# Optimization experiments

Hardware: AMD Instinct MI355X
Metric: run time of the kernel (lower is better)

## Reference

```python
import jax, jax.numpy as jnp
import numpy as np

B, T, D = 2, 2048, 1024
H = 16
HD = D // H
WINDOW = 128
N_GLOBAL = 1
SCALE = 1.0 / np.sqrt(HD)


def _attend_mask(T):
    # True = allowed to attend: banded local window + global rows/cols
    idx = jnp.arange(T)
    dist = jnp.abs(idx[:, None] - idx[None, :])
    attend = dist <= WINDOW
    glb = idx < N_GLOBAL
    attend = attend | glb[:, None] | glb[None, :]
    return attend  # [T, T] bool


def setup_inputs() -> dict:
    key = jax.random.key(0)
    ks = jax.random.split(key, 5)
    scale_w = 1.0 / np.sqrt(D)
    return {
        "x": jax.random.normal(ks[0], (B, T, D), dtype=jnp.float32),
        "Wq": jax.random.normal(ks[1], (D, D), dtype=jnp.float32) * scale_w,
        "Wk": jax.random.normal(ks[2], (D, D), dtype=jnp.float32) * scale_w,
        "Wv": jax.random.normal(ks[3], (D, D), dtype=jnp.float32) * scale_w,
        "Wo": jax.random.normal(ks[4], (D, D), dtype=jnp.float32) * scale_w,
    }


def reference(x, Wq, Wk, Wv, Wo):
    Bb, Tt, Dd = x.shape
    # torch nn.Linear: y = x @ W.T
    q = (x @ Wq.T).reshape(Bb, Tt, H, HD).transpose(0, 2, 1, 3)  # [B,H,T,hd]
    k = (x @ Wk.T).reshape(Bb, Tt, H, HD).transpose(0, 2, 1, 3)
    v = (x @ Wv.T).reshape(Bb, Tt, H, HD).transpose(0, 2, 1, 3)

    attend = _attend_mask(Tt)  # [T,T]
    logits = jnp.einsum("bhqd,bhkd->bhqk", q, k) * SCALE
    logits = jnp.where(attend[None, None, :, :], logits, -jnp.inf)
    weights = jax.nn.softmax(logits, axis=-1)
    weights = jnp.nan_to_num(weights)
    out = jnp.einsum("bhqk,bhkd->bhqd", weights, v)
    out = out.transpose(0, 2, 1, 3).reshape(Bb, Tt, Dd)
    return out @ Wo.T
```

## Files before the change

### kernel.cpp

```cpp
#include <hip/hip_runtime.h>

typedef unsigned short u16;
typedef __attribute__((ext_vector_type(8))) __bf16 bf16x8;
typedef __attribute__((ext_vector_type(4))) float f32x4;
typedef __attribute__((ext_vector_type(8))) u16 u16x8;

#define T_SEQ 2048
#define DIM   1024
#define HDIM  64
#define WIN   128
#define XN_EL (2 * T_SEQ * DIM)

#define AS1 __attribute__((address_space(1)))
#define AS3 __attribute__((address_space(3)))

__device__ __forceinline__ u16 f2bf(float f) {
  union { float f; unsigned u; } v; v.f = f;
  unsigned r = v.u + 0x7fffu + ((v.u >> 16) & 1u);
  return (u16)(r >> 16);
}
__device__ __forceinline__ float bf2f(u16 u) {
  union { unsigned u; float f; } v; v.u = ((unsigned)u) << 16; return v.f;
}
__device__ __forceinline__ void bar() {
  asm volatile("" ::: "memory");
  __builtin_amdgcn_s_barrier();
  asm volatile("" ::: "memory");
}

__global__ __launch_bounds__(256) void cvt_all(
    const float* __restrict__ x,  const float* __restrict__ wq,
    const float* __restrict__ wk, const float* __restrict__ wv,
    const float* __restrict__ wo, u16* __restrict__ xb, u16* __restrict__ wb) {
  const int bid = blockIdx.x;
  const float* s;
  u16* d;
  int off;
  if (bid < 2048) {
    s = x; d = xb; off = bid * 2048;
  } else {
    const int w = bid - 2048;
    const int m = w >> 9;
    s = (m == 0) ? wq : ((m == 1) ? wk : ((m == 2) ? wv : wo));
    d = wb + ((size_t)m << 20);
    off = (w & 511) * 2048;
  }
  const int i = off + threadIdx.x * 8;
  const float4* s4 = (const float4*)(s + i);
  float4 a = s4[0], b = s4[1];
  u16x8 r;
  r[0] = f2bf(a.x); r[1] = f2bf(a.y); r[2] = f2bf(a.z); r[3] = f2bf(a.w);
  r[4] = f2bf(b.x); r[5] = f2bf(b.y); r[6] = f2bf(b.z); r[7] = f2bf(b.w);
  *(u16x8*)(d + i) = r;
}

template <int BM, int BN, int WM, int WN, int OS, int SPLIT, typename OUT_T>
__global__ __launch_bounds__(WM * WN * 64, 2) void gemm3(
    const u16* __restrict__ A, const u16* __restrict__ B,
    OUT_T* __restrict__ C, int nbm) {
  constexpr int NW = WM * WN;
  constexpr int RM = BM / WM, RN = BN / WN;
  constexpr int MF = RM / 16, NF = RN / 16;
  constexpr int MPH = MF / 4;
  constexpr int NT = DIM / 64;
  constexpr int CA = BM / 8, CB = BN / 8;
  constexpr int ANW = CA / NW;
  constexpr int BNW = CB / NW;

  __shared__ u16 As[2][BM * 64];
  __shared__ u16 Bs[2][BN * 64];

  const int tid = threadIdx.x;
  const int lane = tid & 63;
  const int wid = tid >> 6;
  const int wr = wid / WN, wc = wid % WN;
  const int c15 = lane & 15, g = lane >> 4;
  const int lr = lane >> 3;
  const int lcs = ((lane & 7) ^ lr) << 3;

  const int cpx = gridDim.x >> 3;
  const int bid = ((int)blockIdx.x & 7) * cpx + ((int)blockIdx.x >> 3);
  const int bm = bid % nbm;
  const int nb = bid / nbm;
  const u16* Ab = A + (size_t)bm * BM * DIM;
  const u16* Bb = B + (size_t)nb * BN * DIM;

  f32x4 acc[MF][NF];
#pragma unroll
  for (int m = 0; m < MF; ++m)
#pragma unroll
    for (int n = 0; n < NF; ++n) acc[m][n] = (f32x4){0.f, 0.f, 0.f, 0.f};

  auto stA = [&](int buf, int half, int k0) {
#pragma unroll
    for (int i = 0; i < ANW / 2; ++i) {
      const int c = half * (CA / 2) + wid * (ANW / 2) + i;
      __builtin_amdgcn_global_load_lds(
          (const AS1 void*)(Ab + (size_t)(c * 8 + lr) * DIM + k0 + lcs),
          (AS3 void*)(&As[buf][c * 512]), 16, 0, 0);
    }
  };
  auto stB = [&](int buf, int k0) {
#pragma unroll
    for (int i = 0; i < BNW; ++i) {
      const int c = wid * BNW + i;
      __builtin_amdgcn_global_load_lds(
          (const AS1 void*)(Bb + (size_t)(c * 8 + lr) * DIM + k0 + lcs),
          (AS3 void*)(&Bs[buf][c * 512]), 16, 0, 0);
    }
  };

  stA(0, 0, 0); stA(0, 1, 0);
  stB(0, 0); stB(1, 64);
  if constexpr (BNW == 3) asm volatile("s_waitcnt vmcnt(3)" ::: "memory");
  else                    asm volatile("s_waitcnt vmcnt(4)" ::: "memory");
  bar();

  for (int t = 0; t < NT; ++t) {
    const int buf = t & 1;
    const int k0 = t * 64;
    bf16x8 bfrag[NF][2];
#pragma unroll
    for (int p = 0; p < 4; ++p) {
      if (p == 0) {
#pragma unroll
        for (int n = 0; n < NF; ++n)
#pragma unroll
          for (int ks = 0; ks < 2; ++ks) {
            const int r = wc * RN + n * 16 + c15;
            bfrag[n][ks] = *(const bf16x8*)(
                &Bs[buf][r * 64 + ((ks * 32 + g * 8) ^ ((r & 7) << 3))]);
          }
      }
      bf16x8 af[MPH][2];
#pragma unroll
      for (int m = 0; m < MPH; ++m)
#pragma unroll
        for (int ks = 0; ks < 2; ++ks) {
          const int r = wr * RM + (p * MPH + m) * 16 + c15;
          af[m][ks] = *(const bf16x8*)(
              &As[buf][r * 64 + ((ks * 32 + g * 8) ^ ((r & 7) << 3))]);
        }
      if (p == 0) {
        if (t + 1 < NT) stA(buf ^ 1, 0, k0 + 64);
      } else if (p == 1) {
        if (t + 1 < NT) stA(buf ^ 1, 1, k0 + 64);
      } else if (p == 2) {
        if (t + 2 < NT) stB(buf, k0 + 128);
      } else {
        if (t < NT - 2) {
          if constexpr (BNW == 3) asm volatile("s_waitcnt vmcnt(3)" ::: "memory");
          else                    asm volatile("s_waitcnt vmcnt(4)" ::: "memory");
        } else {
          asm volatile("s_waitcnt vmcnt(0)" ::: "memory");
        }
      }
      bar();
      __builtin_amdgcn_s_setprio(1);
#pragma unroll
      for (int m = 0; m < MPH; ++m)
#pragma unroll
        for (int n = 0; n < NF; ++n)
#pragma unroll
          for (int ks = 0; ks < 2; ++ks)
            acc[p * MPH + m][n] = __builtin_amdgcn_mfma_f32_16x16x32_bf16(
                af[m][ks], bfrag[n][ks], acc[p * MPH + m][n], 0, 0, 0);
      __builtin_amdgcn_s_setprio(0);
      bar();
    }
  }

#pragma unroll
  for (int m = 0; m < MF; ++m) {
    const int row0 = bm * BM + wr * RM + m * 16 + g * 4;
#pragma unroll
    for (int n = 0; n < NF; ++n) {
      const int col = nb * BN + wc * RN + n * 16 + c15;
#pragma unroll
      for (int j = 0; j < 4; ++j) {
        if constexpr (SPLIT) {
          u16* dst = (u16*)C + (size_t)(col >> 10) * (size_t)XN_EL +
                     (col & 1023) + (size_t)(row0 + j) * DIM;
          *dst = f2bf(acc[m][n][j]);
        } else {
          const size_t idx = (size_t)(row0 + j) * OS + col;
          if constexpr (sizeof(OUT_T) == 2) C[idx] = f2bf(acc[m][n][j]);
          else C[idx] = acc[m][n][j];
        }
      }
    }
  }
}

__global__ __launch_bounds__(256) void sparse_attn(
    const u16* __restrict__ Q, const u16* __restrict__ K,
    const u16* __restrict__ V, u16* __restrict__ AO) {
  __shared__ u16 Ks[64 * 72];
  __shared__ u16 Vt[64 * 72];
  __shared__ u16 Pl[4][16 * 72];
  __shared__ float Pg[4][16];

  const int tid = threadIdx.x;
  const int lane = tid & 63;
  const int wid = tid >> 6;
  const size_t ha = (size_t)blockIdx.z * T_SEQ * DIM + (size_t)blockIdx.y * HDIM;
  const u16* Qp = Q + ha;
  const u16* Kp = K + ha;
  const u16* Vp = V + ha;

  if (blockIdx.x == 32) {
    float* qs   = (float*)Pg;
    float* ps   = (float*)Ks;
    float* rbuf = (float*)Vt;
    float* red  = (float*)Pl;

    if (tid < HDIM) qs[tid] = bf2f(Qp[tid]);
    __syncthreads();

    float lsum = 0.f;
#pragma unroll
    for (int j = 0; j < 8; ++j) {
      const int k = tid + 256 * j;
      const u16* kr = Kp + (size_t)k * DIM;
      float acc = 0.f;
#pragma unroll
      for (int d0 = 0; d0 < 8; ++d0) {
        u16x8 kv = *(const u16x8*)(kr + d0 * 8);
#pragma unroll
        for (int e = 0; e < 8; ++e) acc += qs[d0 * 8 + e] * bf2f(kv[e]);
      }
      const float p = __expf(acc * 0.125f);
      ps[k] = p;
      lsum += p;
    }
#pragma unroll
    for (int s = 1; s < 64; s <<= 1) lsum += __shfl_xor(lsum, s);
    if (lane == 0) red[wid] = lsum;
    __syncthreads();
    const float denom = red[0] + red[1] + red[2] + red[3];

    const int kg = tid >> 3, dg = tid & 7;
    float facc[8] = {0.f, 0.f, 0.f, 0.f, 0.f, 0.f, 0.f, 0.f};
#pragma unroll 8
    for (int i = 0; i < 64; ++i) {
      const int k = kg * 64 + i;
      const u16x8 vv = *(const u16x8*)(Vp + (size_t)k * DIM + dg * 8);
      const float p = ps[k];
#pragma unroll
      for (int e = 0; e < 8; ++e) facc[e] += p * bf2f(vv[e]);
    }
#pragma unroll
    for (int e = 0; e < 8; ++e) rbuf[kg * 64 + dg * 8 + e] = facc[e];
    __syncthreads();
    if (tid < HDIM) {
      float tot = 0.f;
#pragma unroll
      for (int k2 = 0; k2 < 32; ++k2) tot += rbuf[k2 * 64 + tid];
      AO[ha + tid] = f2bf(tot / denom);
    }
    return;
  }

  const int c15 = lane & 15;
  const int g = lane >> 4;
  const int q0 = blockIdx.x * 64;

  bf16x8 qf0, qf1;
  {
    const u16* qp = Qp + (size_t)(q0 + wid * 16 + c15) * DIM + g * 8;
    qf0 = *(const bf16x8*)qp;
    qf1 = *(const bf16x8*)(qp + 32);
  }

  float lrun[4] = {0.f, 0.f, 0.f, 0.f};
  f32x4 ao[4];
#pragma unroll
  for (int c = 0; c < 4; ++c) ao[c] = (f32x4){0.f, 0.f, 0.f, 0.f};

  const int klo = (q0 > WIN) ? (q0 - WIN) : 0;
  int khi = q0 + 64 + WIN;
  if (khi > T_SEQ) khi = T_SEQ;
  const int nt = (khi - klo) >> 6;

  const int srr = tid >> 2;
  const int scc = (tid & 3) * 16;
  const int vr = srr ^ ((scc >> 4) << 4);

  const u16* kbase = Kp + (size_t)(klo + srr) * DIM + scc;
  const u16* vbase = Vp + (size_t)(klo + srr) * DIM + scc;
  u16x8 kp0 = *(const u16x8*)kbase;
  u16x8 kp1 = *(const u16x8*)(kbase + 8);
  u16x8 vp0 = *(const u16x8*)vbase;
  u16x8 vp1 = *(const u16x8*)(vbase + 8);

  for (int ti = 0; ti < nt; ++ti) {
    const int kt = klo + ti * 64;
    *(u16x8*)(Ks + srr * 72 + scc) = kp0;
    *(u16x8*)(Ks + srr * 72 + scc + 8) = kp1;
#pragma unroll
    for (int e = 0; e < 8; ++e) {
      Vt[(scc + e) * 72 + vr] = vp0[e];
      Vt[(scc + 8 + e) * 72 + vr] = vp1[e];
    }
    __syncthreads();

    if (ti + 1 < nt) {
      const u16* kn = kbase + (size_t)(ti + 1) * 64 * DIM;
      const u16* vn = vbase + (size_t)(ti + 1) * 64 * DIM;
      kp0 = *(const u16x8*)kn;
      kp1 = *(const u16x8*)(kn + 8);
      vp0 = *(const u16x8*)vn;
      vp1 = *(const u16x8*)(vn + 8);
    }

    f32x4 s[4];
#pragma unroll
    for (int t = 0; t < 4; ++t) {
      const u16* kr = Ks + (t * 16 + c15) * 72 + g * 8;
      bf16x8 ka = *(const bf16x8*)kr;
      bf16x8 kb = *(const bf16x8*)(kr + 32);
      s[t] = (f32x4){0.f, 0.f, 0.f, 0.f};
      s[t] = __builtin_amdgcn_mfma_f32_16x16x32_bf16(qf0, ka, s[t], 0, 0, 0);
      s[t] = __builtin_amdgcn_mfma_f32_16x16x32_bf16(qf1, kb, s[t], 0, 0, 0);
    }
#pragma unroll
    for (int j = 0; j < 4; ++j) {
      const int qg = q0 + wid * 16 + g * 4 + j;
#pragma unroll
      for (int t = 0; t < 4; ++t) {
        const int kg = kt + t * 16 + c15;
        const int dd = qg - kg;
        const bool ok = (kg == 0) || (dd <= WIN && dd >= -WIN);
        const float p = ok ? __expf(s[t][j] * 0.125f) : 0.f;
        lrun[j] += p;
        Pl[wid][(g * 4 + j) * 72 + t * 16 + c15] = f2bf(p);
      }
    }
    asm volatile("s_waitcnt lgkmcnt(0)" ::: "memory");

    const bf16x8 pa0 = *(const bf16x8*)(&Pl[wid][c15 * 72 + g * 8]);
    const bf16x8 pa1 = *(const bf16x8*)(&Pl[wid][c15 * 72 + 32 + g * 8]);
#pragma unroll
    for (int c = 0; c < 4; ++c) {
      const int rb = (c * 16 + c15) * 72;
      bf16x8 va = *(const bf16x8*)(Vt + rb + ((g * 8) ^ (c << 4)));
      bf16x8 vb = *(const bf16x8*)(Vt + rb + ((32 + g * 8) ^ (c << 4)));
      ao[c] = __builtin_amdgcn_mfma_f32_16x16x32_bf16(pa0, va, ao[c], 0, 0, 0);
      ao[c] = __builtin_amdgcn_mfma_f32_16x16x32_bf16(pa1, vb, ao[c], 0, 0, 0);
    }
    __syncthreads();
  }

  float ltot[4];
#pragma unroll
  for (int j = 0; j < 4; ++j) {
    float ls = lrun[j];
    ls += __shfl_xor(ls, 1);
    ls += __shfl_xor(ls, 2);
    ls += __shfl_xor(ls, 4);
    ls += __shfl_xor(ls, 8);
    ltot[j] = ls;
  }

  if (klo > 0) {
    const u16x8 qu0 = *(const u16x8*)&qf0;
    const u16x8 qu1 = *(const u16x8*)&qf1;
    const u16x8 k0a = *(const u16x8*)(Kp + g * 8);
    const u16x8 k0b = *(const u16x8*)(Kp + 32 + g * 8);
    float sg = 0.f;
#pragma unroll
    for (int e = 0; e < 8; ++e)
      sg += bf2f(qu0[e]) * bf2f(k0a[e]) + bf2f(qu1[e]) * bf2f(k0b[e]);
    sg += __shfl_xor(sg, 16);
    sg += __shfl_xor(sg, 32);
    const float pg = __expf(sg * 0.125f);
    Pg[wid][c15] = pg;
    asm volatile("s_waitcnt lgkmcnt(0)" ::: "memory");
#pragma unroll
    for (int j = 0; j < 4; ++j) {
      const float pj = Pg[wid][g * 4 + j];
      ltot[j] += pj;
#pragma unroll
      for (int c = 0; c < 4; ++c)
        ao[c][j] += pj * bf2f(Vp[c * 16 + c15]);
    }
  }

#pragma unroll
  for (int j = 0; j < 4; ++j) {
    const int qrow = q0 + wid * 16 + g * 4 + j;
    if (qrow == 0) continue;
    const float inv = 1.0f / ltot[j];
#pragma unroll
    for (int c = 0; c < 4; ++c)
      AO[ha + (size_t)qrow * DIM + c * 16 + c15] = f2bf(ao[c][j] * inv);
  }
}

extern "C" void kernel_launch(void* const* d_in, const int* in_sizes, int n_in,
                              void* d_out, int out_size, void* d_ws, size_t ws_size,
                              hipStream_t stream) {
  const float* x  = (const float*)d_in[0];
  const float* Wq = (const float*)d_in[1];
  const float* Wk = (const float*)d_in[2];
  const float* Wv = (const float*)d_in[3];
  const float* Wo = (const float*)d_in[4];
  float* out = (float*)d_out;

  const int WN = DIM * DIM;

  u16* ws  = (u16*)d_ws;
  u16* xb  = ws;
  u16* wb  = ws + (size_t)XN_EL;
  u16* Wob = wb + (size_t)3 * WN;
  u16* Qb  = wb + (size_t)4 * WN;
  u16* Kb  = Qb + (size_t)XN_EL;
  u16* Vb  = Kb + (size_t)XN_EL;

  cvt_all<<<4096, 256, 0, stream>>>(x, Wq, Wk, Wv, Wo, xb, wb);

  gemm3<256, 192, 2, 4, DIM, 1, u16><<<256, 512, 0, stream>>>(xb, wb, Qb, 16);

  sparse_attn<<<dim3(33, 16, 2), 256, 0, stream>>>(Qb, Kb, Vb, xb);

  gemm3<128, 128, 2, 2, DIM, 0, float><<<256, 256, 0, stream>>>(xb, Wob, out, 32);
}
```

Before: 106.6 us.

## Write V transposed from QKV GEMM and double-buffer attention tiles via direct LDS loads

The QKV GEMM epilogue now writes V head-transposed ([b,h,d,t]), so the attention kernel no longer transposes V through scalar LDS stores. K and V tiles are staged with global_load_lds into double-buffered, XOR-swizzled LDS, which replaces the register prefetch. A fast path skips the mask computation for tiles that lie fully inside the window. The global-row reduction is reworked to read the transposed V. The risks are more LDS use, a stride-T scattered epilogue store for V, and a swizzle that has to match between the direct-load and read patterns.

```diff
diff --git a/kernel.cpp b/kernel.cpp
--- a/kernel.cpp
+++ b/kernel.cpp
@@ -4,6 +4,7 @@
 typedef __attribute__((ext_vector_type(8))) __bf16 bf16x8;
 typedef __attribute__((ext_vector_type(4))) float f32x4;
 typedef __attribute__((ext_vector_type(8))) u16 u16x8;
+typedef __attribute__((ext_vector_type(4))) u16 u16x4;
 
 #define T_SEQ 2048
 #define DIM   1024
@@ -176,13 +177,26 @@
 #pragma unroll
     for (int n = 0; n < NF; ++n) {
       const int col = nb * BN + wc * RN + n * 16 + c15;
-#pragma unroll
-      for (int j = 0; j < 4; ++j) {
-        if constexpr (SPLIT) {
-          u16* dst = (u16*)C + (size_t)(col >> 10) * (size_t)XN_EL +
-                     (col & 1023) + (size_t)(row0 + j) * DIM;
-          *dst = f2bf(acc[m][n][j]);
+      if constexpr (SPLIT) {
+        if (col < 2048) {
+#pragma unroll
+          for (int j = 0; j < 4; ++j) {
+            u16* dst = (u16*)C + (size_t)(col >> 10) * (size_t)XN_EL +
+                       (col & 1023) + (size_t)(row0 + j) * DIM;
+            *dst = f2bf(acc[m][n][j]);
+          }
         } else {
+          const int h = (col - 2048) >> 6, dd = (col - 2048) & 63;
+          u16x4 pk;
+#pragma unroll
+          for (int j = 0; j < 4; ++j) pk[j] = f2bf(acc[m][n][j]);
+          const size_t vidx =
+              ((size_t)((row0 >> 11) * 16 + h) * 64 + dd) * T_SEQ + (row0 & 2047);
+          *(u16x4*)((u16*)C + (size_t)2 * XN_EL + vidx) = pk;
+        }
+      } else {
+#pragma unroll
+        for (int j = 0; j < 4; ++j) {
           const size_t idx = (size_t)(row0 + j) * OS + col;
           if constexpr (sizeof(OUT_T) == 2) C[idx] = f2bf(acc[m][n][j]);
           else C[idx] = acc[m][n][j];
@@ -194,9 +208,9 @@
 
 __global__ __launch_bounds__(256) void sparse_attn(
     const u16* __restrict__ Q, const u16* __restrict__ K,
-    const u16* __restrict__ V, u16* __restrict__ AO) {
-  __shared__ u16 Ks[64 * 72];
-  __shared__ u16 Vt[64 * 72];
+    const u16* __restrict__ VT, u16* __restrict__ AO) {
+  __shared__ u16 Kt[2][64 * 64];
+  __shared__ u16 Vt[2][64 * 64];
   __shared__ u16 Pl[4][16 * 72];
   __shared__ float Pg[4][16];
 
@@ -204,15 +218,16 @@
   const int lane = tid & 63;
   const int wid = tid >> 6;
   const size_t ha = (size_t)blockIdx.z * T_SEQ * DIM + (size_t)blockIdx.y * HDIM;
+  const size_t hv = ((size_t)blockIdx.z * 16 + blockIdx.y) * HDIM * T_SEQ;
   const u16* Qp = Q + ha;
   const u16* Kp = K + ha;
-  const u16* Vp = V + ha;
+  const u16* Vp = VT + hv;
 
   if (blockIdx.x == 32) {
-    float* qs   = (float*)Pg;
-    float* ps   = (float*)Ks;
-    float* rbuf = (float*)Vt;
-    float* red  = (float*)Pl;
+    float* qs   = (float*)Pl;
+    float* ps   = (float*)(&Kt[0][0]);
+    float* rbuf = (float*)(&Vt[0][0]);
+    float* red  = (float*)Pg;
 
     if (tid < HDIM) qs[tid] = bf2f(Qp[tid]);
     __syncthreads();
@@ -239,23 +254,19 @@
     __syncthreads();
     const float denom = red[0] + red[1] + red[2] + red[3];
 
-    const int kg = tid >> 3, dg = tid & 7;
-    float facc[8] = {0.f, 0.f, 0.f, 0.f, 0.f, 0.f, 0.f, 0.f};
-#pragma unroll 8
-    for (int i = 0; i < 64; ++i) {
-      const int k = kg * 64 + i;
-      const u16x8 vv = *(const u16x8*)(Vp + (size_t)k * DIM + dg * 8);
-      const float p = ps[k];
-#pragma unroll
-      for (int e = 0; e < 8; ++e) facc[e] += p * bf2f(vv[e]);
-    }
-#pragma unroll
-    for (int e = 0; e < 8; ++e) rbuf[kg * 64 + dg * 8 + e] = facc[e];
+    const int d = tid & 63, kc = tid >> 6;
+    const u16* vr = Vp + (size_t)d * T_SEQ + kc * 512;
+    float facc = 0.f;
+#pragma unroll 4
+    for (int i = 0; i < 512; i += 8) {
+      const u16x8 vv = *(const u16x8*)(vr + i);
+#pragma unroll
+      for (int e = 0; e < 8; ++e) facc += ps[kc * 512 + i + e] * bf2f(vv[e]);
+    }
+    rbuf[kc * 64 + d] = facc;
     __syncthreads();
     if (tid < HDIM) {
-      float tot = 0.f;
-#pragma unroll
-      for (int k2 = 0; k2 < 32; ++k2) tot += rbuf[k2 * 64 + tid];
+      const float tot = rbuf[tid] + rbuf[64 + tid] + rbuf[128 + tid] + rbuf[192 + tid];
       AO[ha + tid] = f2bf(tot / denom);
     }
     return;
@@ -282,58 +293,64 @@
   if (khi > T_SEQ) khi = T_SEQ;
   const int nt = (khi - klo) >> 6;
 
-  const int srr = tid >> 2;
-  const int scc = (tid & 3) * 16;
-  const int vr = srr ^ ((scc >> 4) << 4);
-
-  const u16* kbase = Kp + (size_t)(klo + srr) * DIM + scc;
-  const u16* vbase = Vp + (size_t)(klo + srr) * DIM + scc;
-  u16x8 kp0 = *(const u16x8*)kbase;
-  u16x8 kp1 = *(const u16x8*)(kbase + 8);
-  u16x8 vp0 = *(const u16x8*)vbase;
-  u16x8 vp1 = *(const u16x8*)(vbase + 8);
+  const int lr = lane >> 3;
+  const int lcs = ((lane & 7) ^ lr) << 3;
+
+  auto stage = [&](int buf, int kt) {
+#pragma unroll
+    for (int i = 0; i < 2; ++i) {
+      const int c = wid * 2 + i;
+      __builtin_amdgcn_global_load_lds(
+          (const AS1 void*)(Kp + (size_t)(kt + c * 8 + lr) * DIM + lcs),
+          (AS3 void*)(&Kt[buf][c * 512]), 16, 0, 0);
+      __builtin_amdgcn_global_load_lds(
+          (const AS1 void*)(Vp + (size_t)(c * 8 + lr) * T_SEQ + kt + lcs),
+          (AS3 void*)(&Vt[buf][c * 512]), 16, 0, 0);
+    }
+  };
+
+  stage(0, klo);
+  asm volatile("s_waitcnt vmcnt(0)" ::: "memory");
+  __syncthreads();
 
   for (int ti = 0; ti < nt; ++ti) {
     const int kt = klo + ti * 64;
-    *(u16x8*)(Ks + srr * 72 + scc) = kp0;
-    *(u16x8*)(Ks + srr * 72 + scc + 8) = kp1;
-#pragma unroll
-    for (int e = 0; e < 8; ++e) {
-      Vt[(scc + e) * 72 + vr] = vp0[e];
-      Vt[(scc + 8 + e) * 72 + vr] = vp1[e];
-    }
-    __syncthreads();
-
-    if (ti + 1 < nt) {
-      const u16* kn = kbase + (size_t)(ti + 1) * 64 * DIM;
-      const u16* vn = vbase + (size_t)(ti + 1) * 64 * DIM;
-      kp0 = *(const u16x8*)kn;
-      kp1 = *(const u16x8*)(kn + 8);
-      vp0 = *(const u16x8*)vn;
-      vp1 = *(const u16x8*)(vn + 8);
-    }
+    const int buf = ti & 1;
+    if (ti + 1 < nt) stage(buf ^ 1, kt + 64);
 
     f32x4 s[4];
 #pragma unroll
     for (int t = 0; t < 4; ++t) {
-      const u16* kr = Ks + (t * 16 + c15) * 72 + g * 8;
-      bf16x8 ka = *(const bf16x8*)kr;
-      bf16x8 kb = *(const bf16x8*)(kr + 32);
+      const int r = t * 16 + c15;
+      bf16x8 ka = *(const bf16x8*)(&Kt[buf][r * 64 + ((g * 8) ^ ((r & 7) << 3))]);
+      bf16x8 kb = *(const bf16x8*)(&Kt[buf][r * 64 + ((32 + g * 8) ^ ((r & 7) << 3))]);
       s[t] = (f32x4){0.f, 0.f, 0.f, 0.f};
       s[t] = __builtin_amdgcn_mfma_f32_16x16x32_bf16(qf0, ka, s[t], 0, 0, 0);
       s[t] = __builtin_amdgcn_mfma_f32_16x16x32_bf16(qf1, kb, s[t], 0, 0, 0);
     }
-#pragma unroll
-    for (int j = 0; j < 4; ++j) {
-      const int qg = q0 + wid * 16 + g * 4 + j;
-#pragma unroll
-      for (int t = 0; t < 4; ++t) {
-        const int kg = kt + t * 16 + c15;
-        const int dd = qg - kg;
-        const bool ok = (kg == 0) || (dd <= WIN && dd >= -WIN);
-        const float p = ok ? __expf(s[t][j] * 0.125f) : 0.f;
-        lrun[j] += p;
-        Pl[wid][(g * 4 + j) * 72 + t * 16 + c15] = f2bf(p);
+    if (kt >= q0 - 65 && kt <= q0 + 65) {
+#pragma unroll
+      for (int j = 0; j < 4; ++j) {
+#pragma unroll
+        for (int t = 0; t < 4; ++t) {
+          const float p = __expf(s[t][j] * 0.125f);
+          lrun[j] += p;
+          Pl[wid][(g * 4 + j) * 72 + t * 16 + c15] = f2bf(p);
+        }
+      }
+    } else {
+#pragma unroll
+      for (int j = 0; j < 4; ++j) {
+        const int qg = q0 + wid * 16 + g * 4 + j;
+#pragma unroll
+        for (int t = 0; t < 4; ++t) {
+          const int kg = kt + t * 16 + c15;
+          const int dd = qg - kg;
+          const bool ok = (kg == 0) || (dd <= WIN && dd >= -WIN);
+          const float p = ok ? __expf(s[t][j] * 0.125f) : 0.f;
+          lrun[j] += p;
+          Pl[wid][(g * 4 + j) * 72 + t * 16 + c15] = f2bf(p);
+        }
       }
     }
     asm volatile("s_waitcnt lgkmcnt(0)" ::: "memory");
@@ -342,9 +359,9 @@
     const bf16x8 pa1 = *(const bf16x8*)(&Pl[wid][c15 * 72 + 32 + g * 8]);
 #pragma unroll
     for (int c = 0; c < 4; ++c) {
-      const int rb = (c * 16 + c15) * 72;
-      bf16x8 va = *(const bf16x8*)(Vt + rb + ((g * 8) ^ (c << 4)));
-      bf16x8 vb = *(const bf16x8*)(Vt + rb + ((32 + g * 8) ^ (c << 4)));
+      const int r = c * 16 + c15;
+      bf16x8 va = *(const bf16x8*)(&Vt[buf][r * 64 + ((g * 8) ^ ((r & 7) << 3))]);
+      bf16x8 vb = *(const bf16x8*)(&Vt[buf][r * 64 + ((32 + g * 8) ^ ((r & 7) << 3))]);
       ao[c] = __builtin_amdgcn_mfma_f32_16x16x32_bf16(pa0, va, ao[c], 0, 0, 0);
       ao[c] = __builtin_amdgcn_mfma_f32_16x16x32_bf16(pa1, vb, ao[c], 0, 0, 0);
     }
@@ -382,7 +399,7 @@
       ltot[j] += pj;
 #pragma unroll
       for (int c = 0; c < 4; ++c)
-        ao[c][j] += pj * bf2f(Vp[c * 16 + c15]);
+        ao[c][j] += pj * bf2f(Vp[(size_t)(c * 16 + c15) * T_SEQ]);
     }
   }
 
@@ -415,13 +432,13 @@
   u16* Wob = wb + (size_t)3 * WN;
   u16* Qb  = wb + (size_t)4 * WN;
   u16* Kb  = Qb + (size_t)XN_EL;
-  u16* Vb  = Kb + (size_t)XN_EL;
+  u16* VTb = Qb + (size_t)2 * XN_EL;
 
   cvt_all<<<4096, 256, 0, stream>>>(x, Wq, Wk, Wv, Wo, xb, wb);
 
   gemm3<256, 192, 2, 4, DIM, 1, u16><<<256, 512, 0, stream>>>(xb, wb, Qb, 16);
 
-  sparse_attn<<<dim3(33, 16, 2), 256, 0, stream>>>(Qb, Kb, Vb, xb);
+  sparse_attn<<<dim3(33, 16, 2), 256, 0, stream>>>(Qb, Kb, VTb, xb);
 
   gemm3<128, 128, 2, 2, DIM, 0, float><<<256, 256, 0, stream>>>(xb, Wob, out, 32);
 }
```

New measurement: 114.7 us. +7.6%, slower.

## Process 128 query rows per attention block and skip masking on interior tiles

Applied to the files above, without the earlier changes.

Each attention block now covers 128 queries instead of 64, with every wave handling two 16-row groups. Each staged K/V tile in shared memory is therefore reused by twice as many queries, which cuts redundant global loads of the overlapping window. The grid shrinks from 33 to 17 blocks per head. A fast path also drops the per-element mask test when the tile lies entirely inside the band. The cost is fewer blocks, and so less parallelism and latency hiding, plus higher register pressure from the doubled accumulators.

```diff
diff --git a/kernel.cpp b/kernel.cpp
--- a/kernel.cpp
+++ b/kernel.cpp
@@ -198,7 +198,7 @@
   __shared__ u16 Ks[64 * 72];
   __shared__ u16 Vt[64 * 72];
   __shared__ u16 Pl[4][16 * 72];
-  __shared__ float Pg[4][16];
+  __shared__ float Pg[4][32];
 
   const int tid = threadIdx.x;
   const int lane = tid & 63;
@@ -208,11 +208,11 @@
   const u16* Kp = K + ha;
   const u16* Vp = V + ha;
 
-  if (blockIdx.x == 32) {
-    float* qs   = (float*)Pg;
+  if (blockIdx.x == 16) {
+    float* qs   = (float*)(&Pl[0][0]);
     float* ps   = (float*)Ks;
     float* rbuf = (float*)Vt;
-    float* red  = (float*)Pl;
+    float* red  = (float*)Pg;
 
     if (tid < HDIM) qs[tid] = bf2f(Qp[tid]);
     __syncthreads();
@@ -263,28 +263,35 @@
 
   const int c15 = lane & 15;
   const int g = lane >> 4;
-  const int q0 = blockIdx.x * 64;
-
-  bf16x8 qf0, qf1;
+  const int q0 = blockIdx.x * 128;
+  const int qw = q0 + wid * 32;
+
+  bf16x8 qA0, qA1, qB0, qB1;
   {
-    const u16* qp = Qp + (size_t)(q0 + wid * 16 + c15) * DIM + g * 8;
-    qf0 = *(const bf16x8*)qp;
-    qf1 = *(const bf16x8*)(qp + 32);
-  }
-
-  float lrun[4] = {0.f, 0.f, 0.f, 0.f};
-  f32x4 ao[4];
-#pragma unroll
-  for (int c = 0; c < 4; ++c) ao[c] = (f32x4){0.f, 0.f, 0.f, 0.f};
+    const u16* qp = Qp + (size_t)(qw + c15) * DIM + g * 8;
+    qA0 = *(const bf16x8*)qp;
+    qA1 = *(const bf16x8*)(qp + 32);
+    const u16* qp2 = qp + 16 * DIM;
+    qB0 = *(const bf16x8*)qp2;
+    qB1 = *(const bf16x8*)(qp2 + 32);
+  }
+
+  float lrA[4] = {0.f, 0.f, 0.f, 0.f}, lrB[4] = {0.f, 0.f, 0.f, 0.f};
+  f32x4 aoA[4], aoB[4];
+#pragma unroll
+  for (int c = 0; c < 4; ++c) {
+    aoA[c] = (f32x4){0.f, 0.f, 0.f, 0.f};
+    aoB[c] = (f32x4){0.f, 0.f, 0.f, 0.f};
+  }
 
   const int klo = (q0 > WIN) ? (q0 - WIN) : 0;
-  int khi = q0 + 64 + WIN;
+  int khi = q0 + 128 + WIN;
   if (khi > T_SEQ) khi = T_SEQ;
   const int nt = (khi - klo) >> 6;
 
   const int srr = tid >> 2;
   const int scc = (tid & 3) * 16;
-  const int vr = srr ^ ((scc >> 4) << 4);
+  const int vr = srr ^ (scc & 48);
 
   const u16* kbase = Kp + (size_t)(klo + srr) * DIM + scc;
   const u16* vbase = Vp + (size_t)(klo + srr) * DIM + scc;
@@ -313,87 +320,119 @@
       vp1 = *(const u16x8*)(vn + 8);
     }
 
-    f32x4 s[4];
-#pragma unroll
-    for (int t = 0; t < 4; ++t) {
-      const u16* kr = Ks + (t * 16 + c15) * 72 + g * 8;
-      bf16x8 ka = *(const bf16x8*)kr;
-      bf16x8 kb = *(const bf16x8*)(kr + 32);
-      s[t] = (f32x4){0.f, 0.f, 0.f, 0.f};
-      s[t] = __builtin_amdgcn_mfma_f32_16x16x32_bf16(qf0, ka, s[t], 0, 0, 0);
-      s[t] = __builtin_amdgcn_mfma_f32_16x16x32_bf16(qf1, kb, s[t], 0, 0, 0);
-    }
-#pragma unroll
-    for (int j = 0; j < 4; ++j) {
-      const int qg = q0 + wid * 16 + g * 4 + j;
+    auto do_group = [&](const bf16x8& qf0, const bf16x8& qf1, int r0,
+                        float* lrun, f32x4* ao) {
+      f32x4 s[4];
 #pragma unroll
       for (int t = 0; t < 4; ++t) {
-        const int kg = kt + t * 16 + c15;
-        const int dd = qg - kg;
-        const bool ok = (kg == 0) || (dd <= WIN && dd >= -WIN);
-        const float p = ok ? __expf(s[t][j] * 0.125f) : 0.f;
-        lrun[j] += p;
-        Pl[wid][(g * 4 + j) * 72 + t * 16 + c15] = f2bf(p);
-      }
-    }
-    asm volatile("s_waitcnt lgkmcnt(0)" ::: "memory");
-
-    const bf16x8 pa0 = *(const bf16x8*)(&Pl[wid][c15 * 72 + g * 8]);
-    const bf16x8 pa1 = *(const bf16x8*)(&Pl[wid][c15 * 72 + 32 + g * 8]);
-#pragma unroll
-    for (int c = 0; c < 4; ++c) {
-      const int rb = (c * 16 + c15) * 72;
-      bf16x8 va = *(const bf16x8*)(Vt + rb + ((g * 8) ^ (c << 4)));
-      bf16x8 vb = *(const bf16x8*)(Vt + rb + ((32 + g * 8) ^ (c << 4)));
-      ao[c] = __builtin_amdgcn_mfma_f32_16x16x32_bf16(pa0, va, ao[c], 0, 0, 0);
-      ao[c] = __builtin_amdgcn_mfma_f32_16x16x32_bf16(pa1, vb, ao[c], 0, 0, 0);
-    }
+        const u16* kr = Ks + (t * 16 + c15) * 72 + g * 8;
+        bf16x8 ka = *(const bf16x8*)kr;
+        bf16x8 kb = *(const bf16x8*)(kr + 32);
+        f32x4 z = (f32x4){0.f, 0.f, 0.f, 0.f};
+        z = __builtin_amdgcn_mfma_f32_16x16x32_bf16(qf0, ka, z, 0, 0, 0);
+        s[t] = __builtin_amdgcn_mfma_f32_16x16x32_bf16(qf1, kb, z, 0, 0, 0);
+      }
+      if (kt >= r0 - 113 && kt <= r0 + 65) {
+#pragma unroll
+        for (int j = 0; j < 4; ++j) {
+#pragma unroll
+          for (int t = 0; t < 4; ++t) {
+            const float p = __expf(s[t][j] * 0.125f);
+            lrun[j] += p;
+            Pl[wid][(g * 4 + j) * 72 + t * 16 + c15] = f2bf(p);
+          }
+        }
+      } else {
+#pragma unroll
+        for (int j = 0; j < 4; ++j) {
+          const int qg = r0 + g * 4 + j;
+#pragma unroll
+          for (int t = 0; t < 4; ++t) {
+            const int kg = kt + t * 16 + c15;
+            const int dd = qg - kg;
+            const bool ok = (kg == 0) || (dd <= WIN && dd >= -WIN);
+            const float p = ok ? __expf(s[t][j] * 0.125f) : 0.f;
+            lrun[j] += p;
+            Pl[wid][(g * 4 + j) * 72 + t * 16 + c15] = f2bf(p);
+          }
+        }
+      }
+      asm volatile("s_waitcnt lgkmcnt(0)" ::: "memory");
+
+      const bf16x8 pa0 = *(const bf16x8*)(&Pl[wid][c15 * 72 + g * 8]);
+      const bf16x8 pa1 = *(const bf16x8*)(&Pl[wid][c15 * 72 + 32 + g * 8]);
+#pragma unroll
+      for (int c = 0; c < 4; ++c) {
+        const int rb = (c * 16 + c15) * 72;
+        bf16x8 va = *(const bf16x8*)(Vt + rb + ((g * 8) ^ (c << 4)));
+        bf16x8 vb = *(const bf16x8*)(Vt + rb + ((32 + g * 8) ^ (c << 4)));
+        ao[c] = __builtin_amdgcn_mfma_f32_16x16x32_bf16(pa0, va, ao[c], 0, 0, 0);
+        ao[c] = __builtin_amdgcn_mfma_f32_16x16x32_bf16(pa1, vb, ao[c], 0, 0, 0);
+      }
+    };
+
+    do_group(qA0, qA1, qw, lrA, aoA);
+    do_group(qB0, qB1, qw + 16, lrB, aoB);
+
     __syncthreads();
   }
 
-  float ltot[4];
+  float ltA[4], ltB[4];
 #pragma unroll
   for (int j = 0; j < 4; ++j) {
-    float ls = lrun[j];
-    ls += __shfl_xor(ls, 1);
-    ls += __shfl_xor(ls, 2);
-    ls += __shfl_xor(ls, 4);
-    ls += __shfl_xor(ls, 8);
-    ltot[j] = ls;
+    float a = lrA[j], b = lrB[j];
+    a += __shfl_xor(a, 1); b += __shfl_xor(b, 1);
+    a += __shfl_xor(a, 2); b += __shfl_xor(b, 2);
+    a += __shfl_xor(a, 4); b += __shfl_xor(b, 4);
+    a += __shfl_xor(a, 8); b += __shfl_xor(b, 8);
+    ltA[j] = a; ltB[j] = b;
   }
 
   if (klo > 0) {
-    const u16x8 qu0 = *(const u16x8*)&qf0;
-    const u16x8 qu1 = *(const u16x8*)&qf1;
     const u16x8 k0a = *(const u16x8*)(Kp + g * 8);
     const u16x8 k0b = *(const u16x8*)(Kp + 32 + g * 8);
-    float sg = 0.f;
-#pragma unroll
-    for (int e = 0; e < 8; ++e)
-      sg += bf2f(qu0[e]) * bf2f(k0a[e]) + bf2f(qu1[e]) * bf2f(k0b[e]);
-    sg += __shfl_xor(sg, 16);
-    sg += __shfl_xor(sg, 32);
-    const float pg = __expf(sg * 0.125f);
-    Pg[wid][c15] = pg;
+    const u16x8 qa0 = *(const u16x8*)&qA0;
+    const u16x8 qa1 = *(const u16x8*)&qA1;
+    const u16x8 qb0 = *(const u16x8*)&qB0;
+    const u16x8 qb1 = *(const u16x8*)&qB1;
+    float sgA = 0.f, sgB = 0.f;
+#pragma unroll
+    for (int e = 0; e < 8; ++e) {
+      sgA += bf2f(qa0[e]) * bf2f(k0a[e]) + bf2f(qa1[e]) * bf2f(k0b[e]);
+      sgB += bf2f(qb0[e]) * bf2f(k0a[e]) + bf2f(qb1[e]) * bf2f(k0b[e]);
+    }
+    sgA += __shfl_xor(sgA, 16); sgA += __shfl_xor(sgA, 32);
+    sgB += __shfl_xor(sgB, 16); sgB += __shfl_xor(sgB, 32);
+    Pg[wid][c15] = __expf(sgA * 0.125f);
+    Pg[wid][16 + c15] = __expf(sgB * 0.125f);
     asm volatile("s_waitcnt lgkmcnt(0)" ::: "memory");
 #pragma unroll
     for (int j = 0; j < 4; ++j) {
-      const float pj = Pg[wid][g * 4 + j];
-      ltot[j] += pj;
-#pragma unroll
-      for (int c = 0; c < 4; ++c)
-        ao[c][j] += pj * bf2f(Vp[c * 16 + c15]);
+      const float pA = Pg[wid][g * 4 + j];
+      const float pB = Pg[wid][16 + g * 4 + j];
+      ltA[j] += pA;
+      ltB[j] += pB;
+#pragma unroll
+      for (int c = 0; c < 4; ++c) {
+        const float v0 = bf2f(Vp[c * 16 + c15]);
+        aoA[c][j] += pA * v0;
+        aoB[c][j] += pB * v0;
+      }
     }
   }
 
 #pragma unroll
   for (int j = 0; j < 4; ++j) {
-    const int qrow = q0 + wid * 16 + g * 4 + j;
-    if (qrow == 0) continue;
-    const float inv = 1.0f / ltot[j];
-#pragma unroll
-    for (int c = 0; c < 4; ++c)
-      AO[ha + (size_t)qrow * DIM + c * 16 + c15] = f2bf(ao[c][j] * inv);
+    const int qrA = qw + g * 4 + j;
+    const int qrB = qrA + 16;
+    const float invA = 1.0f / ltA[j];
+    const float invB = 1.0f / ltB[j];
+#pragma unroll
+    for (int c = 0; c < 4; ++c) {
+      if (qrA != 0)
+        AO[ha + (size_t)qrA * DIM + c * 16 + c15] = f2bf(aoA[c][j] * invA);
+      AO[ha + (size_t)qrB * DIM + c * 16 + c15] = f2bf(aoB[c][j] * invB);
+    }
   }
 }
 
@@ -421,7 +460,7 @@
 
   gemm3<256, 192, 2, 4, DIM, 1, u16><<<256, 512, 0, stream>>>(xb, wb, Qb, 16);
 
-  sparse_attn<<<dim3(33, 16, 2), 256, 0, stream>>>(Qb, Kb, Vb, xb);
+  sparse_attn<<<dim3(17, 16, 2), 256, 0, stream>>>(Qb, Kb, Vb, xb);
 
   gemm3<128, 128, 2, 2, DIM, 0, float><<<256, 256, 0, stream>>>(xb, Wob, out, 32);
 }
```

Result: faster. 104.4 us (-2.1%).
